# Performance work log

Hardware: AMD Instinct MI355X
Metric: run time of the kernel (lower is better)

The kernel has to match this reference:

```python
import jax, jax.numpy as jnp
import numpy as np

B, C, N, H = 4, 256, 1024, 8
D = C // H
EPS = 1e-5

def setup_inputs() -> dict:
    key = jax.random.key(0)
    ks = jax.random.split(key, 10)
    s = lambda k, shape: (jax.random.normal(k, shape, jnp.float32) * 0.02)
    return dict(
        node_embeds=jax.random.normal(ks[0], (B, C, N), jnp.float32),
        edge_embeds=jax.random.normal(ks[1], (B, N, N), jnp.float32),
        da_prior=jax.random.normal(ks[2], (B, N, C), jnp.float32),
        gamma=jnp.ones((C,), jnp.float32),
        beta=jnp.zeros((C,), jnp.float32),
        w_qkv=s(ks[3], (C, 3 * C)),            # Linear(node_dim, 3*node_dim), no bias
        w_proj=s(ks[4], (C, C)),
        b_proj=jnp.zeros((C,), jnp.float32),
        w_expand=s(ks[5], (H,)),               # Conv2d(1,H,1) weight (per-head scalar)
        b_expand=jnp.zeros((H,), jnp.float32),
        w_reduce=s(ks[6], (H,)),               # Conv2d(H,1,1) weight
        b_reduce=jnp.zeros((1,), jnp.float32),
        w_fc=s(ks[7], (1, C)),                 # Linear(edge_dim=1, node_dim)
        b_fc=jnp.zeros((C,), jnp.float32),
    )

def reference(node_embeds, edge_embeds, da_prior, gamma, beta, w_qkv,
              w_proj, b_proj, w_expand, b_expand, w_reduce, b_reduce, w_fc, b_fc):
    x = jnp.swapaxes(node_embeds, 1, 2)                       # [B,N,C]
    # einsum 'bnn,bnc->bnc': diagonal of edge matrix scales each node
    diag = jnp.diagonal(edge_embeds, axis1=1, axis2=2)        # [B,N]
    attned = diag[:, :, None] * x                             # [B,N,C]
    # einsum 'bnc,bca->bnc' with prior permuted [B,C,A]: multiply by sum over A
    prior_sum = da_prior.sum(axis=1)                          # [B,C]
    x = attned * prior_sum[:, None, :] + x                    # residual add
    # LayerNorm over channel dim
    mu = x.mean(-1, keepdims=True)
    var = x.var(-1, keepdims=True)
    ln = (x - mu) * jax.lax.rsqrt(var + EPS) * gamma + beta
    qkv = (ln @ w_qkv).reshape(B, N, 3, H, D)
    q = jnp.transpose(qkv[:, :, 0], (0, 2, 1, 3))             # [B,H,N,D]
    k = jnp.transpose(qkv[:, :, 1], (0, 2, 1, 3))
    v = jnp.transpose(qkv[:, :, 2], (0, 2, 1, 3))
    scale = D ** -0.5
    attn = jnp.einsum('bhnd,bhmd->bhnm', q, k) * scale        # [B,H,N,N]
    bias = edge_embeds[:, None] * w_expand[None, :, None, None] + b_expand[None, :, None, None]
    attn = attn + bias                                        # pre-softmax scores = residual
    a = jax.nn.softmax(attn, axis=-1)
    node = jnp.einsum('bhnm,bhmd->bnhd', a, v).reshape(B, N, C)
    # reduce conv over heads on (softmax + residual)
    edge = jnp.einsum('bhnm,h->bnm', a + attn, w_reduce) + b_reduce[0]  # [B,N,N]
    w = jax.nn.softmax(edge, axis=-1)
    wsum = (w * edge).sum(-1)                                 # [B,N]
    node = node + wsum[:, :, None] @ w_fc + b_fc              # fc: [B,N,1]@[1,C]
    node = node @ w_proj + b_proj
    return jnp.swapaxes(node, 1, 2), edge                     # ([B,C,N], [B,N,N])
```

## Files before the change

### kernel.cpp

```cpp
#include <hip/hip_runtime.h>
#include <math.h>

#define Bn 4
#define Cn 256
#define Nn 1024
#define Hn 8
#define Dn 32
#define BHND (Bn * Hn * Nn * Dn)
#define BHN  (Bn * Hn * Nn)

typedef short bf16x8 __attribute__((ext_vector_type(8)));
typedef float f32x4 __attribute__((ext_vector_type(4)));

__device__ inline unsigned f2bf_rn_bits(float x) {
  union { float f; unsigned u; } v; v.f = x;
  return (v.u + 0x7FFFu + ((v.u >> 16) & 1u)) >> 16;
}
__device__ inline float bfbits2f(unsigned b) {
  union { unsigned u; float f; } v; v.u = b << 16; return v.f;
}
__device__ inline void split_bf(float x, unsigned& hi, unsigned& lo) {
  hi = f2bf_rn_bits(x);
  lo = f2bf_rn_bits(x - bfbits2f(hi));
}
__device__ inline unsigned split_bf_trunc_pack(float x) {
  union { float f; unsigned u; } v; v.f = x;
  unsigned hi = v.u >> 16;
  union { unsigned u; float f; } hv; hv.u = hi << 16;
  union { float f; unsigned u; } r; r.f = x - hv.f;
  return hi | (r.u & 0xffff0000u);
}
__device__ inline void split4(const float4& a, float sc, short4& hs, short4& ls) {
  unsigned hb, lb;
  split_bf(a.x * sc, hb, lb); hs.x = (short)hb; ls.x = (short)lb;
  split_bf(a.y * sc, hb, lb); hs.y = (short)hb; ls.y = (short)lb;
  split_bf(a.z * sc, hb, lb); hs.z = (short)hb; ls.z = (short)lb;
  split_bf(a.w * sc, hb, lb); hs.w = (short)hb; ls.w = (short)lb;
}
__device__ inline void unpack_u32x8(const uint4& a, const uint4& b, bf16x8& hi, bf16x8& lo) {
  int4 h4, l4;
  h4.x = (int)((a.x & 0xffffu) | (a.y << 16));  l4.x = (int)((a.x >> 16) | (a.y & 0xffff0000u));
  h4.y = (int)((a.z & 0xffffu) | (a.w << 16));  l4.y = (int)((a.z >> 16) | (a.w & 0xffff0000u));
  h4.z = (int)((b.x & 0xffffu) | (b.y << 16));  l4.z = (int)((b.x >> 16) | (b.y & 0xffff0000u));
  h4.w = (int)((b.z & 0xffffu) | (b.w << 16));  l4.w = (int)((b.z >> 16) | (b.w & 0xffff0000u));
  hi = *(bf16x8*)&h4; lo = *(bf16x8*)&l4;
}

__global__ __launch_bounds__(256) void k_prior_part(const float* __restrict__ dap,
                                                    float* __restrict__ pp) {
  int bi = blockIdx.x;
  int b = bi >> 5, ch = bi & 31;
  int c = threadIdx.x;
  float s = 0.f;
  int n0 = ch * 32;
  for (int n = n0; n < n0 + 32; ++n) s += dap[(size_t)(b * Nn + n) * Cn + c];
  pp[(size_t)(b * 32 + ch) * Cn + c] = s;
}

__global__ __launch_bounds__(256) void k_prior_red(const float* __restrict__ pp,
                                                   float* __restrict__ prior) {
  int i = blockIdx.x * 256 + threadIdx.x;
  int b = i >> 8, c = i & 255;
  float s = 0.f;
  for (int ch = 0; ch < 32; ++ch) s += pp[(size_t)(b * 32 + ch) * Cn + c];
  prior[i] = s;
}

__global__ __launch_bounds__(256) void k_transpose(const float* __restrict__ ne,
                                                   float* __restrict__ xw) {
  __shared__ float tile[32][33];
  int bi = blockIdx.x;
  int b = bi >> 8, rem = bi & 255;
  int c0 = (rem >> 5) << 5;
  int n0 = (rem & 31) << 5;
  int tx = threadIdx.x & 31, ty = threadIdx.x >> 5;
#pragma unroll
  for (int i = 0; i < 4; ++i) {
    int c = c0 + ty + i * 8;
    tile[ty + i * 8][tx] = ne[(size_t)(b * Cn + c) * Nn + n0 + tx];
  }
  __syncthreads();
#pragma unroll
  for (int i = 0; i < 4; ++i) {
    int n = n0 + ty + i * 8;
    xw[(size_t)(b * Nn + n) * Cn + c0 + tx] = tile[tx][ty + i * 8];
  }
}

__global__ __launch_bounds__(256) void k_prep_ln(const float* __restrict__ xw,
                                                 const float* __restrict__ eg,
                                                 const float* __restrict__ prior,
                                                 const float* __restrict__ gamma,
                                                 const float* __restrict__ beta,
                                                 float* __restrict__ ln) {
  int bn = blockIdx.x;
  int b = bn >> 10, n = bn & 1023;
  int c = threadIdx.x;
  float x = xw[(size_t)bn * Cn + c];
  float dg = eg[(size_t)(b * Nn + n) * Nn + n];
  float x2 = x * (1.f + dg * prior[b * Cn + c]);
  float s = x2, qq = x2 * x2;
#pragma unroll
  for (int off = 32; off >= 1; off >>= 1) {
    s += __shfl_xor(s, off);
    qq += __shfl_xor(qq, off);
  }
  __shared__ float ss[4], sq[4];
  if ((c & 63) == 0) { ss[c >> 6] = s; sq[c >> 6] = qq; }
  __syncthreads();
  s = ss[0] + ss[1] + ss[2] + ss[3];
  qq = sq[0] + sq[1] + sq[2] + sq[3];
  float mu = s * (1.f / 256.f);
  float var = qq * (1.f / 256.f) - mu * mu;
  float r = rsqrtf(var + 1e-5f);
  ln[(size_t)bn * Cn + c] = (x2 - mu) * r * gamma[c] + beta[c];
}

__global__ __launch_bounds__(256) void k_qkv_gemm(const float* __restrict__ ln,
                                                  const float* __restrict__ wqkv,
                                                  short* __restrict__ q_hi,
                                                  short* __restrict__ q_lo,
                                                  short* __restrict__ k_hi,
                                                  short* __restrict__ k_lo,
                                                  short* __restrict__ vt_hi,
                                                  short* __restrict__ vt_lo) {
  __shared__ __align__(16) float at[16][68];
  __shared__ __align__(16) float bt[16][68];
  __shared__ float ct[64][65];
  int m0 = blockIdx.x * 64;
  int j0 = blockIdx.y * 64;
  int t = threadIdx.x;
  int tx = t & 15, ty = t >> 4;
  float4 acc[4] = {};
  for (int k0 = 0; k0 < 256; k0 += 16) {
    {
      int row = t >> 2, k4 = (t & 3) << 2;
      float4 a = *(const float4*)&ln[(size_t)(m0 + row) * 256 + k0 + k4];
      at[k4 + 0][row] = a.x; at[k4 + 1][row] = a.y;
      at[k4 + 2][row] = a.z; at[k4 + 3][row] = a.w;
      int rb = t >> 4, jb = (t & 15) << 2;
      *(float4*)&bt[rb][jb] = *(const float4*)&wqkv[(size_t)(k0 + rb) * 768 + j0 + jb];
    }
    __syncthreads();
#pragma unroll
    for (int kk = 0; kk < 16; ++kk) {
      float4 a4 = *(float4*)&at[kk][ty << 2];
      float4 b4 = *(float4*)&bt[kk][tx << 2];
      acc[0].x += a4.x * b4.x; acc[0].y += a4.x * b4.y; acc[0].z += a4.x * b4.z; acc[0].w += a4.x * b4.w;
      acc[1].x += a4.y * b4.x; acc[1].y += a4.y * b4.y; acc[1].z += a4.y * b4.z; acc[1].w += a4.y * b4.w;
      acc[2].x += a4.z * b4.x; acc[2].y += a4.z * b4.y; acc[2].z += a4.z * b4.z; acc[2].w += a4.z * b4.w;
      acc[3].x += a4.w * b4.x; acc[3].y += a4.w * b4.y; acc[3].z += a4.w * b4.z; acc[3].w += a4.w * b4.w;
    }
    __syncthreads();
  }
  int b = m0 >> 10, n0 = m0 & 1023;
  int three = (j0 + (tx << 2)) >> 8;
  const float scale = 0.17677669529663687f;
  if (three == 2) {
#pragma unroll
    for (int i = 0; i < 4; ++i) {
      ct[(ty << 2) + i][(tx << 2) + 0] = acc[i].x;
      ct[(ty << 2) + i][(tx << 2) + 1] = acc[i].y;
      ct[(ty << 2) + i][(tx << 2) + 2] = acc[i].z;
      ct[(ty << 2) + i][(tx << 2) + 3] = acc[i].w;
    }
    __syncthreads();
    int jl = t >> 2;
    int n4 = (t & 3) * 16;
    int rem = (j0 & 255) + jl;
    int h = rem >> 5, d = rem & 31;
    short hs[16], ls[16];
#pragma unroll
    for (int u = 0; u < 16; ++u) {
      unsigned hb, lb;
      split_bf(ct[n4 + u][jl], hb, lb);
      hs[u] = (short)hb; ls[u] = (short)lb;
    }
    size_t ob = ((size_t)(b * Hn + h) * Dn + d) * Nn + n0 + n4;
    *(uint4*)&vt_hi[ob] = *(uint4*)&hs[0];
    *(uint4*)&vt_hi[ob + 8] = *(uint4*)&hs[8];
    *(uint4*)&vt_lo[ob] = *(uint4*)&ls[0];
    *(uint4*)&vt_lo[ob + 8] = *(uint4*)&ls[8];
  } else {
    int j = j0 + (tx << 2);
    int rem = j & 255, h = rem >> 5, dd = rem & 31;
    short* dst_hi = (three == 0) ? q_hi : k_hi;
    short* dst_lo = (three == 0) ? q_lo : k_lo;
    float sc = (three == 0) ? 1.0f : scale;
#pragma unroll
    for (int i = 0; i < 4; ++i) {
      int m = m0 + (ty << 2) + i;
      int bb = m >> 10, n = m & 1023;
      size_t base = (size_t)((bb * Hn + h) * Nn + n) * Dn + dd;
      short4 hs, ls; split4(acc[i], sc, hs, ls);
      *(short4*)&dst_hi[base] = hs; *(short4*)&dst_lo[base] = ls;
    }
  }
}

__global__ __launch_bounds__(256, 4) void k_attn_core(
    const short* __restrict__ q_hi, const short* __restrict__ q_lo,
    const short* __restrict__ k_hi, const short* __restrict__ k_lo,
    const short* __restrict__ vt_hi, const short* __restrict__ vt_lo,
    const float* __restrict__ eg,
    const float* __restrict__ w_expand, const float* __restrict__ b_expand,
    float* __restrict__ o_part, float* __restrict__ l_part) {
  __shared__ short kh[64 * 40];
  __shared__ short kl[64 * 40];
  __shared__ short vth[32 * 72];
  __shared__ short vtl[32 * 72];
  __shared__ unsigned pbuf[4][16 * 68];

  int blk = blockIdx.x;
  int mh = blk & 1;
  int nt = (blk >> 1) & 15;
  int h = (blk >> 5) & 7;
  int b = blk >> 8;
  int n0 = nt * 64;
  int t = threadIdx.x, wid = t >> 6, l = t & 63;
  int lr = l & 15, lq = l >> 4;

  const float we = w_expand[h], be = b_expand[h];
  size_t bhb = (size_t)(b * Hn + h) * Nn * Dn;
  const short* khg = k_hi + bhb;
  const short* klg = k_lo + bhb;
  const short* vhg = vt_hi + bhb;
  const short* vlg = vt_lo + bhb;

  bf16x8 qhi, qlo;
  {
    size_t qoff = bhb + (size_t)(n0 + wid * 16 + lr) * Dn + lq * 8;
    qhi = *(const bf16x8*)&q_hi[qoff];
    qlo = *(const bf16x8*)&q_lo[qoff];
  }

  f32x4 O0 = {0.f, 0.f, 0.f, 0.f}, O1 = {0.f, 0.f, 0.f, 0.f};
  float rowsum[4] = {0.f, 0.f, 0.f, 0.f};
  int nrow = n0 + wid * 16 + lq * 4;

  for (int ms = 0; ms < 8; ++ms) {
    int m0 = mh * 512 + ms * 64;
    float eb[4][4];
#pragma unroll
    for (int reg = 0; reg < 4; ++reg) {
      const float* ep = &eg[(size_t)(b * Nn + nrow + reg) * Nn + m0 + lr];
#pragma unroll
      for (int msub = 0; msub < 4; ++msub) eb[msub][reg] = ep[msub * 16];
    }
    __syncthreads();
    {
      int row = t >> 2, c = (t & 3) * 8;
      *(uint4*)&kh[row * 40 + c] = *(const uint4*)&khg[(size_t)(m0 + row) * Dn + c];
      *(uint4*)&kl[row * 40 + c] = *(const uint4*)&klg[(size_t)(m0 + row) * Dn + c];
      int d = t >> 3, cm = (t & 7) * 8;
      *(uint4*)&vth[d * 72 + cm] = *(const uint4*)&vhg[(size_t)d * Nn + m0 + cm];
      *(uint4*)&vtl[d * 72 + cm] = *(const uint4*)&vlg[(size_t)d * Nn + m0 + cm];
    }
    __syncthreads();

#pragma unroll
    for (int msub = 0; msub < 4; ++msub) {
      int mrow = msub * 16 + lr;
      bf16x8 bh8 = *(bf16x8*)&kh[mrow * 40 + lq * 8];
      bf16x8 bl8 = *(bf16x8*)&kl[mrow * 40 + lq * 8];
      f32x4 sacc = {0.f, 0.f, 0.f, 0.f};
      sacc = __builtin_amdgcn_mfma_f32_16x16x32_bf16(qlo, bh8, sacc, 0, 0, 0);
      sacc = __builtin_amdgcn_mfma_f32_16x16x32_bf16(qhi, bl8, sacc, 0, 0, 0);
      sacc = __builtin_amdgcn_mfma_f32_16x16x32_bf16(qhi, bh8, sacc, 0, 0, 0);
#pragma unroll
      for (int reg = 0; reg < 4; ++reg) {
        float s = sacc[reg] + eb[msub][reg] * we + be;
        float e = __expf(s);
        rowsum[reg] += e;
        pbuf[wid][(lq * 4 + reg) * 68 + msub * 16 + lr] = split_bf_trunc_pack(e);
      }
    }

#pragma unroll
    for (int mw = 0; mw < 2; ++mw) {
      uint4 pa = *(uint4*)&pbuf[wid][lr * 68 + mw * 32 + lq * 8];
      uint4 pb = *(uint4*)&pbuf[wid][lr * 68 + mw * 32 + lq * 8 + 4];
      bf16x8 ahi, alo;
      unpack_u32x8(pa, pb, ahi, alo);
      {
        bf16x8 vh8 = *(bf16x8*)&vth[lr * 72 + mw * 32 + lq * 8];
        bf16x8 vl8 = *(bf16x8*)&vtl[lr * 72 + mw * 32 + lq * 8];
        O0 = __builtin_amdgcn_mfma_f32_16x16x32_bf16(alo, vh8, O0, 0, 0, 0);
        O0 = __builtin_amdgcn_mfma_f32_16x16x32_bf16(ahi, vl8, O0, 0, 0, 0);
        O0 = __builtin_amdgcn_mfma_f32_16x16x32_bf16(ahi, vh8, O0, 0, 0, 0);
      }
      {
        bf16x8 vh8 = *(bf16x8*)&vth[(16 + lr) * 72 + mw * 32 + lq * 8];
        bf16x8 vl8 = *(bf16x8*)&vtl[(16 + lr) * 72 + mw * 32 + lq * 8];
        O1 = __builtin_amdgcn_mfma_f32_16x16x32_bf16(alo, vh8, O1, 0, 0, 0);
        O1 = __builtin_amdgcn_mfma_f32_16x16x32_bf16(ahi, vl8, O1, 0, 0, 0);
        O1 = __builtin_amdgcn_mfma_f32_16x16x32_bf16(ahi, vh8, O1, 0, 0, 0);
      }
    }
  }

#pragma unroll
  for (int reg = 0; reg < 4; ++reg) {
#pragma unroll
    for (int off = 1; off < 16; off <<= 1)
      rowsum[reg] += __shfl_xor(rowsum[reg], off);
  }
  size_t pbase = (size_t)mh * BHND + bhb;
#pragma unroll
  for (int reg = 0; reg < 4; ++reg) {
    int n = nrow + reg;
    o_part[pbase + (size_t)n * Dn + lr] = O0[reg];
    o_part[pbase + (size_t)n * Dn + 16 + lr] = O1[reg];
    if (lr == 0)
      l_part[(size_t)mh * BHN + (size_t)(b * Hn + h) * Nn + n] = rowsum[reg];
  }
}

__global__ __launch_bounds__(256) void k_stats(const float* __restrict__ l_part,
                                               float* __restrict__ stats) {
  int i = blockIdx.x * 256 + threadIdx.x;
  stats[i] = 1.0f / (l_part[i] + l_part[BHN + i]);
}

__global__ __launch_bounds__(256, 4) void k_edge_mfma(
    const short* __restrict__ q_hi, const short* __restrict__ q_lo,
    const short* __restrict__ k_hi, const short* __restrict__ k_lo,
    const float* __restrict__ eg, const float* __restrict__ stats,
    const float* __restrict__ w_expand, const float* __restrict__ b_expand,
    const float* __restrict__ w_reduce, const float* __restrict__ b_reduce,
    float* __restrict__ edge_out) {
  __shared__ short kh[64 * 40];
  __shared__ short kl[64 * 40];
  int blk = blockIdx.x;
  int mt = blk & 15;
  int nt = (blk >> 4) & 15;
  int b = blk >> 8;
  int n0 = nt * 64, m0 = mt * 64;
  int t = threadIdx.x, wid = t >> 6, l = t & 63;
  int lr = l & 15, lq = l >> 4;
  const float br = b_reduce[0];
  int nrow = n0 + wid * 16 + lq * 4;

  float eacc[4][4], ebias[4][4];
#pragma unroll
  for (int reg = 0; reg < 4; ++reg) {
    const float* ep = &eg[(size_t)(b * Nn + nrow + reg) * Nn + m0 + lr];
#pragma unroll
    for (int msub = 0; msub < 4; ++msub) {
      ebias[msub][reg] = ep[msub * 16];
      eacc[msub][reg] = br;
    }
  }

  for (int h = 0; h < Hn; ++h) {
    size_t bhb = (size_t)(b * Hn + h) * Nn * Dn;
    float we = w_expand[h], be = b_expand[h], wr = w_reduce[h];
    bf16x8 qhi, qlo;
    {
      size_t qoff = bhb + (size_t)(n0 + wid * 16 + lr) * Dn + lq * 8;
      qhi = *(const bf16x8*)&q_hi[qoff];
      qlo = *(const bf16x8*)&q_lo[qoff];
    }
    float invl[4];
#pragma unroll
    for (int reg = 0; reg < 4; ++reg)
      invl[reg] = stats[(size_t)(b * Hn + h) * Nn + nrow + reg];

    __syncthreads();
    {
      int row = t >> 2, c = (t & 3) * 8;
      *(uint4*)&kh[row * 40 + c] = *(const uint4*)&k_hi[bhb + (size_t)(m0 + row) * Dn + c];
      *(uint4*)&kl[row * 40 + c] = *(const uint4*)&k_lo[bhb + (size_t)(m0 + row) * Dn + c];
    }
    __syncthreads();
#pragma unroll
    for (int msub = 0; msub < 4; ++msub) {
      int mrow = msub * 16 + lr;
      bf16x8 bh8 = *(bf16x8*)&kh[mrow * 40 + lq * 8];
      bf16x8 bl8 = *(bf16x8*)&kl[mrow * 40 + lq * 8];
      f32x4 sacc = {0.f, 0.f, 0.f, 0.f};
      sacc = __builtin_amdgcn_mfma_f32_16x16x32_bf16(qlo, bh8, sacc, 0, 0, 0);
      sacc = __builtin_amdgcn_mfma_f32_16x16x32_bf16(qhi, bl8, sacc, 0, 0, 0);
      sacc = __builtin_amdgcn_mfma_f32_16x16x32_bf16(qhi, bh8, sacc, 0, 0, 0);
#pragma unroll
      for (int reg = 0; reg < 4; ++reg) {
        float s = sacc[reg] + ebias[msub][reg] * we + be;
        float p = __expf(s) * invl[reg];
        eacc[msub][reg] += wr * (p + s);
      }
    }
  }
#pragma unroll
  for (int msub = 0; msub < 4; ++msub)
#pragma unroll
    for (int reg = 0; reg < 4; ++reg)
      edge_out[(size_t)(b * Nn + nrow + reg) * Nn + m0 + msub * 16 + lr] = eacc[msub][reg];
}

__global__ __launch_bounds__(256) void k_edge_soft(const float* __restrict__ edge,
                                                   float* __restrict__ wsum) {
  int bn = blockIdx.x;
  int t = threadIdx.x;
  const float* row = edge + (size_t)bn * Nn;
  float4 e = *(const float4*)&row[t * 4];
  float mx = fmaxf(fmaxf(e.x, e.y), fmaxf(e.z, e.w));
#pragma unroll
  for (int off = 32; off >= 1; off >>= 1) mx = fmaxf(mx, __shfl_xor(mx, off));
  __shared__ float sm[4], sl[4], sw[4];
  if ((t & 63) == 0) sm[t >> 6] = mx;
  __syncthreads();
  mx = fmaxf(fmaxf(sm[0], sm[1]), fmaxf(sm[2], sm[3]));
  float p0 = __expf(e.x - mx), p1 = __expf(e.y - mx), p2 = __expf(e.z - mx), p3 = __expf(e.w - mx);
  float ls = p0 + p1 + p2 + p3;
  float ws = p0 * e.x + p1 * e.y + p2 * e.z + p3 * e.w;
#pragma unroll
  for (int off = 32; off >= 1; off >>= 1) { ls += __shfl_xor(ls, off); ws += __shfl_xor(ws, off); }
  if ((t & 63) == 0) { sl[t >> 6] = ls; sw[t >> 6] = ws; }
  __syncthreads();
  if (t == 0) {
    float L = sl[0] + sl[1] + sl[2] + sl[3];
    float Wv = sw[0] + sw[1] + sw[2] + sw[3];
    wsum[bn] = Wv / L;
  }
}

__global__ __launch_bounds__(256) void k_proj_gemm(const float* __restrict__ o_part,
                                                   const float* __restrict__ stats,
                                                   const float* __restrict__ wsum,
                                                   const float* __restrict__ wfc,
                                                   const float* __restrict__ bfc,
                                                   const float* __restrict__ wproj,
                                                   const float* __restrict__ bproj,
                                                   float* __restrict__ out) {
  __shared__ __align__(16) float at[16][68];
  __shared__ __align__(16) float bt[16][68];
  __shared__ float ct[64][65];
  int m0 = blockIdx.x * 64;
  int j0 = blockIdx.y * 64;
  int t = threadIdx.x;
  int tx = t & 15, ty = t >> 4;
  float4 acc[4] = {};
  for (int k0 = 0; k0 < 256; k0 += 16) {
    {
      int row = t >> 2, k4 = (t & 3) << 2;
      int m = m0 + row;
      int bb = m >> 10, n = m & 1023;
      int c = k0 + k4;
      int h = c >> 5, dd = c & 31;
      float wsm = wsum[m];
      size_t ob = ((size_t)(bb * Hn + h) * Nn + n) * Dn + dd;
      float4 oa = *(const float4*)&o_part[ob];
      float4 oc = *(const float4*)&o_part[BHND + ob];
      float inv = stats[(size_t)(bb * Hn + h) * Nn + n];
      float4 a;
      a.x = (oa.x + oc.x) * inv + wsm * wfc[c + 0] + bfc[c + 0];
      a.y = (oa.y + oc.y) * inv + wsm * wfc[c + 1] + bfc[c + 1];
      a.z = (oa.z + oc.z) * inv + wsm * wfc[c + 2] + bfc[c + 2];
      a.w = (oa.w + oc.w) * inv + wsm * wfc[c + 3] + bfc[c + 3];
      at[k4 + 0][row] = a.x; at[k4 + 1][row] = a.y;
      at[k4 + 2][row] = a.z; at[k4 + 3][row] = a.w;
      int rb = t >> 4, jb = (t & 15) << 2;
      *(float4*)&bt[rb][jb] = *(const float4*)&wproj[(size_t)(k0 + rb) * 256 + j0 + jb];
    }
    __syncthreads();
#pragma unroll
    for (int kk = 0; kk < 16; ++kk) {
      float4 a4 = *(float4*)&at[kk][ty << 2];
      float4 b4 = *(float4*)&bt[kk][tx << 2];
      acc[0].x += a4.x * b4.x; acc[0].y += a4.x * b4.y; acc[0].z += a4.x * b4.z; acc[0].w += a4.x * b4.w;
      acc[1].x += a4.y * b4.x; acc[1].y += a4.y * b4.y; acc[1].z += a4.y * b4.z; acc[1].w += a4.y * b4.w;
      acc[2].x += a4.z * b4.x; acc[2].y += a4.z * b4.y; acc[2].z += a4.z * b4.z; acc[2].w += a4.z * b4.w;
      acc[3].x += a4.w * b4.x; acc[3].y += a4.w * b4.y; acc[3].z += a4.w * b4.z; acc[3].w += a4.w * b4.w;
    }
    __syncthreads();
  }
#pragma unroll
  for (int i = 0; i < 4; ++i) {
    ct[(ty << 2) + i][(tx << 2) + 0] = acc[i].x + bproj[j0 + (tx << 2) + 0];
    ct[(ty << 2) + i][(tx << 2) + 1] = acc[i].y + bproj[j0 + (tx << 2) + 1];
    ct[(ty << 2) + i][(tx << 2) + 2] = acc[i].z + bproj[j0 + (tx << 2) + 2];
    ct[(ty << 2) + i][(tx << 2) + 3] = acc[i].w + bproj[j0 + (tx << 2) + 3];
  }
  __syncthreads();
  int b = m0 >> 10, n0 = m0 & 1023;
  int n4 = t & 15, c0i = t >> 4;
#pragma unroll
  for (int u = 0; u < 4; ++u) {
    int ci = c0i + u * 16;
    float4 val = { ct[(n4 << 2) + 0][ci], ct[(n4 << 2) + 1][ci],
                   ct[(n4 << 2) + 2][ci], ct[(n4 << 2) + 3][ci] };
    *(float4*)&out[(size_t)(b * Cn + j0 + ci) * Nn + n0 + (n4 << 2)] = val;
  }
}

extern "C" void kernel_launch(void* const* d_in, const int* in_sizes, int n_in,
                              void* d_out, int out_size, void* d_ws, size_t ws_size,
                              hipStream_t stream) {
  (void)in_sizes; (void)n_in; (void)out_size; (void)ws_size;
  const float* node_embeds = (const float*)d_in[0];
  const float* edge_embeds = (const float*)d_in[1];
  const float* da_prior    = (const float*)d_in[2];
  const float* gamma       = (const float*)d_in[3];
  const float* beta        = (const float*)d_in[4];
  const float* w_qkv       = (const float*)d_in[5];
  const float* w_proj      = (const float*)d_in[6];
  const float* b_proj      = (const float*)d_in[7];
  const float* w_expand    = (const float*)d_in[8];
  const float* b_expand    = (const float*)d_in[9];
  const float* w_reduce    = (const float*)d_in[10];
  const float* b_reduce    = (const float*)d_in[11];
  const float* w_fc        = (const float*)d_in[12];
  const float* b_fc        = (const float*)d_in[13];
  float* out_node = (float*)d_out;
  float* out_edge = out_node + (size_t)Bn * Cn * Nn;

  const size_t M = 1048576;
  float* W = (float*)d_ws;
  float* ws_x   = W;
  float* ws_ln  = W + M;
  float* o_part = W;
  short* vt_hi  = (short*)(W + 2 * M);
  short* vt_lo  = vt_hi + M;
  short* q_hi   = (short*)(W + 3 * M);
  short* q_lo   = q_hi + M;
  short* k_hi   = q_hi + 2 * M;
  short* k_lo   = q_hi + 3 * M;
  float* ws_pp    = W + 5 * M;
  float* ws_prior = ws_pp + Bn * 32 * Cn;
  float* ws_wsum  = ws_prior + Bn * Cn;
  float* ws_stats = ws_wsum + Bn * Nn;
  float* l_part   = ws_stats + BHN;

  k_prior_part<<<dim3(Bn * 32), dim3(256), 0, stream>>>(da_prior, ws_pp);
  k_prior_red<<<dim3(Bn), dim3(256), 0, stream>>>(ws_pp, ws_prior);
  k_transpose<<<dim3(Bn * 256), dim3(256), 0, stream>>>(node_embeds, ws_x);
  k_prep_ln<<<dim3(Bn * Nn), dim3(256), 0, stream>>>(ws_x, edge_embeds, ws_prior,
                                                     gamma, beta, ws_ln);
  k_qkv_gemm<<<dim3(64, 12), dim3(256), 0, stream>>>(ws_ln, w_qkv, q_hi, q_lo,
                                                     k_hi, k_lo, vt_hi, vt_lo);
  k_attn_core<<<dim3(Bn * Hn * 16 * 2), dim3(256), 0, stream>>>(
      q_hi, q_lo, k_hi, k_lo, vt_hi, vt_lo, edge_embeds, w_expand, b_expand,
      o_part, l_part);
  k_stats<<<dim3(BHN / 256), dim3(256), 0, stream>>>(l_part, ws_stats);
  k_edge_mfma<<<dim3(Bn * 16 * 16), dim3(256), 0, stream>>>(
      q_hi, q_lo, k_hi, k_lo, edge_embeds, ws_stats, w_expand, b_expand,
      w_reduce, b_reduce, out_edge);
  k_edge_soft<<<dim3(Bn * Nn), dim3(256), 0, stream>>>(out_edge, ws_wsum);
  k_proj_gemm<<<dim3(64, 4), dim3(256), 0, stream>>>(o_part, ws_stats, ws_wsum,
                                                     w_fc, b_fc, w_proj, b_proj,
                                                     out_node);
}
```

Baseline: 200.2 us.

## Fuse edge softmax into edge kernel, MFMA split-bf16 QKV GEMM, inline stats

The fp32 SIMT QKV GEMM becomes a three-pass split-bf16 MFMA GEMM. LayerNorm now emits hi/lo bf16 directly, and a new pre-kernel transposes and splits w_qkv. The separate edge-softmax pass, which re-read the full edge matrix, is replaced by per-tile exp-sum partials computed in the edge MFMA epilogue, followed by a small reduction kernel. The k_stats kernel is removed and its reciprocal is computed inline where needed. The fused softmax drops the max subtraction, so it could overflow on inputs with large edge values.

Measured after the change: 206.2 us. +3.0%, slower.

```diff
diff --git a/kernel.cpp b/kernel.cpp
--- a/kernel.cpp
+++ b/kernel.cpp
@@ -29,13 +29,6 @@
   union { unsigned u; float f; } hv; hv.u = hi << 16;
   union { float f; unsigned u; } r; r.f = x - hv.f;
   return hi | (r.u & 0xffff0000u);
-}
-__device__ inline void split4(const float4& a, float sc, short4& hs, short4& ls) {
-  unsigned hb, lb;
-  split_bf(a.x * sc, hb, lb); hs.x = (short)hb; ls.x = (short)lb;
-  split_bf(a.y * sc, hb, lb); hs.y = (short)hb; ls.y = (short)lb;
-  split_bf(a.z * sc, hb, lb); hs.z = (short)hb; ls.z = (short)lb;
-  split_bf(a.w * sc, hb, lb); hs.w = (short)hb; ls.w = (short)lb;
 }
 __device__ inline void unpack_u32x8(const uint4& a, const uint4& b, bf16x8& hi, bf16x8& lo) {
   int4 h4, l4;
@@ -87,12 +80,34 @@
   }
 }
 
+__global__ __launch_bounds__(256) void k_split_wt(const float* __restrict__ w,
+                                                  short* __restrict__ wt_h,
+                                                  short* __restrict__ wt_l) {
+  __shared__ float tile[32][33];
+  int bi = blockIdx.x;
+  int j0 = (bi >> 3) << 5;
+  int k0 = (bi & 7) << 5;
+  int tx = threadIdx.x & 31, ty = threadIdx.x >> 5;
+#pragma unroll
+  for (int i = 0; i < 4; ++i)
+    tile[ty + i * 8][tx] = w[(size_t)(k0 + ty + i * 8) * 768 + j0 + tx];
+  __syncthreads();
+#pragma unroll
+  for (int i = 0; i < 4; ++i) {
+    float v = tile[tx][ty + i * 8];
+    unsigned hb, lb; split_bf(v, hb, lb);
+    wt_h[(size_t)(j0 + ty + i * 8) * 256 + k0 + tx] = (short)hb;
+    wt_l[(size_t)(j0 + ty + i * 8) * 256 + k0 + tx] = (short)lb;
+  }
+}
+
 __global__ __launch_bounds__(256) void k_prep_ln(const float* __restrict__ xw,
                                                  const float* __restrict__ eg,
                                                  const float* __restrict__ prior,
                                                  const float* __restrict__ gamma,
                                                  const float* __restrict__ beta,
-                                                 float* __restrict__ ln) {
+                                                 short* __restrict__ ln_h,
+                                                 short* __restrict__ ln_l) {
   int bn = blockIdx.x;
   int b = bn >> 10, n = bn & 1023;
   int c = threadIdx.x;
@@ -113,58 +128,51 @@
   float mu = s * (1.f / 256.f);
   float var = qq * (1.f / 256.f) - mu * mu;
   float r = rsqrtf(var + 1e-5f);
-  ln[(size_t)bn * Cn + c] = (x2 - mu) * r * gamma[c] + beta[c];
-}
-
-__global__ __launch_bounds__(256) void k_qkv_gemm(const float* __restrict__ ln,
-                                                  const float* __restrict__ wqkv,
-                                                  short* __restrict__ q_hi,
-                                                  short* __restrict__ q_lo,
-                                                  short* __restrict__ k_hi,
-                                                  short* __restrict__ k_lo,
-                                                  short* __restrict__ vt_hi,
-                                                  short* __restrict__ vt_lo) {
-  __shared__ __align__(16) float at[16][68];
-  __shared__ __align__(16) float bt[16][68];
+  float v = (x2 - mu) * r * gamma[c] + beta[c];
+  unsigned hb, lb; split_bf(v, hb, lb);
+  ln_h[(size_t)bn * Cn + c] = (short)hb;
+  ln_l[(size_t)bn * Cn + c] = (short)lb;
+}
+
+__global__ __launch_bounds__(256) void k_qkv_mfma(
+    const short* __restrict__ ln_h, const short* __restrict__ ln_l,
+    const short* __restrict__ wt_h, const short* __restrict__ wt_l,
+    short* __restrict__ q_hi, short* __restrict__ q_lo,
+    short* __restrict__ k_hi, short* __restrict__ k_lo,
+    short* __restrict__ vt_hi, short* __restrict__ vt_lo) {
   __shared__ float ct[64][65];
   int m0 = blockIdx.x * 64;
   int j0 = blockIdx.y * 64;
-  int t = threadIdx.x;
-  int tx = t & 15, ty = t >> 4;
-  float4 acc[4] = {};
-  for (int k0 = 0; k0 < 256; k0 += 16) {
-    {
-      int row = t >> 2, k4 = (t & 3) << 2;
-      float4 a = *(const float4*)&ln[(size_t)(m0 + row) * 256 + k0 + k4];
-      at[k4 + 0][row] = a.x; at[k4 + 1][row] = a.y;
-      at[k4 + 2][row] = a.z; at[k4 + 3][row] = a.w;
-      int rb = t >> 4, jb = (t & 15) << 2;
-      *(float4*)&bt[rb][jb] = *(const float4*)&wqkv[(size_t)(k0 + rb) * 768 + j0 + jb];
-    }
-    __syncthreads();
-#pragma unroll
-    for (int kk = 0; kk < 16; ++kk) {
-      float4 a4 = *(float4*)&at[kk][ty << 2];
-      float4 b4 = *(float4*)&bt[kk][tx << 2];
-      acc[0].x += a4.x * b4.x; acc[0].y += a4.x * b4.y; acc[0].z += a4.x * b4.z; acc[0].w += a4.x * b4.w;
-      acc[1].x += a4.y * b4.x; acc[1].y += a4.y * b4.y; acc[1].z += a4.y * b4.z; acc[1].w += a4.y * b4.w;
-      acc[2].x += a4.z * b4.x; acc[2].y += a4.z * b4.y; acc[2].z += a4.z * b4.z; acc[2].w += a4.z * b4.w;
-      acc[3].x += a4.w * b4.x; acc[3].y += a4.w * b4.y; acc[3].z += a4.w * b4.z; acc[3].w += a4.w * b4.w;
-    }
-    __syncthreads();
-  }
+  int t = threadIdx.x, wid = t >> 6, l = t & 63;
+  int lr = l & 15, lq = l >> 4;
+  f32x4 acc[4] = {};
+  const short* ah_p = ln_h + (size_t)(m0 + wid * 16 + lr) * 256 + lq * 8;
+  const short* al_p = ln_l + (size_t)(m0 + wid * 16 + lr) * 256 + lq * 8;
+  const short* bh_p = wt_h + (size_t)(j0 + lr) * 256 + lq * 8;
+  const short* bl_p = wt_l + (size_t)(j0 + lr) * 256 + lq * 8;
+#pragma unroll 2
+  for (int k0 = 0; k0 < 256; k0 += 32) {
+    bf16x8 ah = *(const bf16x8*)&ah_p[k0];
+    bf16x8 al = *(const bf16x8*)&al_p[k0];
+#pragma unroll
+    for (int js = 0; js < 4; ++js) {
+      bf16x8 bh = *(const bf16x8*)&bh_p[js * 16 * 256 + k0];
+      bf16x8 bl = *(const bf16x8*)&bl_p[js * 16 * 256 + k0];
+      acc[js] = __builtin_amdgcn_mfma_f32_16x16x32_bf16(al, bh, acc[js], 0, 0, 0);
+      acc[js] = __builtin_amdgcn_mfma_f32_16x16x32_bf16(ah, bl, acc[js], 0, 0, 0);
+      acc[js] = __builtin_amdgcn_mfma_f32_16x16x32_bf16(ah, bh, acc[js], 0, 0, 0);
+    }
+  }
+#pragma unroll
+  for (int js = 0; js < 4; ++js)
+#pragma unroll
+    for (int reg = 0; reg < 4; ++reg)
+      ct[wid * 16 + lq * 4 + reg][js * 16 + lr] = acc[js][reg];
+  __syncthreads();
   int b = m0 >> 10, n0 = m0 & 1023;
-  int three = (j0 + (tx << 2)) >> 8;
+  int three = j0 >> 8;
   const float scale = 0.17677669529663687f;
   if (three == 2) {
-#pragma unroll
-    for (int i = 0; i < 4; ++i) {
-      ct[(ty << 2) + i][(tx << 2) + 0] = acc[i].x;
-      ct[(ty << 2) + i][(tx << 2) + 1] = acc[i].y;
-      ct[(ty << 2) + i][(tx << 2) + 2] = acc[i].z;
-      ct[(ty << 2) + i][(tx << 2) + 3] = acc[i].w;
-    }
-    __syncthreads();
     int jl = t >> 2;
     int n4 = (t & 3) * 16;
     int rem = (j0 & 255) + jl;
@@ -182,19 +190,25 @@
     *(uint4*)&vt_lo[ob] = *(uint4*)&ls[0];
     *(uint4*)&vt_lo[ob + 8] = *(uint4*)&ls[8];
   } else {
-    int j = j0 + (tx << 2);
-    int rem = j & 255, h = rem >> 5, dd = rem & 31;
-    short* dst_hi = (three == 0) ? q_hi : k_hi;
-    short* dst_lo = (three == 0) ? q_lo : k_lo;
+    int m_l = t & 63, half = t >> 6;
+    int rem = (j0 & 255) + half * 16;
+    int h = rem >> 5, ddb = rem & 31;
+    int n = n0 + m_l;
     float sc = (three == 0) ? 1.0f : scale;
-#pragma unroll
-    for (int i = 0; i < 4; ++i) {
-      int m = m0 + (ty << 2) + i;
-      int bb = m >> 10, n = m & 1023;
-      size_t base = (size_t)((bb * Hn + h) * Nn + n) * Dn + dd;
-      short4 hs, ls; split4(acc[i], sc, hs, ls);
-      *(short4*)&dst_hi[base] = hs; *(short4*)&dst_lo[base] = ls;
-    }
+    short* dh = three ? k_hi : q_hi;
+    short* dl = three ? k_lo : q_lo;
+    short hs[16], ls[16];
+#pragma unroll
+    for (int u = 0; u < 16; ++u) {
+      unsigned hb, lb;
+      split_bf(ct[m_l][half * 16 + u] * sc, hb, lb);
+      hs[u] = (short)hb; ls[u] = (short)lb;
+    }
+    size_t base = ((size_t)((b * Hn + h) * Nn + n)) * Dn + ddb;
+    *(uint4*)&dh[base] = *(uint4*)&hs[0];
+    *(uint4*)&dh[base + 8] = *(uint4*)&hs[8];
+    *(uint4*)&dl[base] = *(uint4*)&ls[0];
+    *(uint4*)&dl[base + 8] = *(uint4*)&ls[8];
   }
 }
 
@@ -316,19 +330,14 @@
   }
 }
 
-__global__ __launch_bounds__(256) void k_stats(const float* __restrict__ l_part,
-                                               float* __restrict__ stats) {
-  int i = blockIdx.x * 256 + threadIdx.x;
-  stats[i] = 1.0f / (l_part[i] + l_part[BHN + i]);
-}
-
 __global__ __launch_bounds__(256, 4) void k_edge_mfma(
     const short* __restrict__ q_hi, const short* __restrict__ q_lo,
     const short* __restrict__ k_hi, const short* __restrict__ k_lo,
-    const float* __restrict__ eg, const float* __restrict__ stats,
+    const float* __restrict__ eg, const float* __restrict__ l_part,
     const float* __restrict__ w_expand, const float* __restrict__ b_expand,
     const float* __restrict__ w_reduce, const float* __restrict__ b_reduce,
-    float* __restrict__ edge_out) {
+    float* __restrict__ edge_out, float* __restrict__ pl_part,
+    float* __restrict__ pwe_part) {
   __shared__ short kh[64 * 40];
   __shared__ short kl[64 * 40];
   int blk = blockIdx.x;
@@ -363,8 +372,10 @@
     }
     float invl[4];
 #pragma unroll
-    for (int reg = 0; reg < 4; ++reg)
-      invl[reg] = stats[(size_t)(b * Hn + h) * Nn + nrow + reg];
+    for (int reg = 0; reg < 4; ++reg) {
+      size_t idx = (size_t)(b * Hn + h) * Nn + nrow + reg;
+      invl[reg] = 1.0f / (l_part[idx] + l_part[BHN + idx]);
+    }
 
     __syncthreads();
     {
@@ -395,37 +406,46 @@
 #pragma unroll
     for (int reg = 0; reg < 4; ++reg)
       edge_out[(size_t)(b * Nn + nrow + reg) * Nn + m0 + msub * 16 + lr] = eacc[msub][reg];
-}
-
-__global__ __launch_bounds__(256) void k_edge_soft(const float* __restrict__ edge,
-                                                   float* __restrict__ wsum) {
-  int bn = blockIdx.x;
-  int t = threadIdx.x;
-  const float* row = edge + (size_t)bn * Nn;
-  float4 e = *(const float4*)&row[t * 4];
-  float mx = fmaxf(fmaxf(e.x, e.y), fmaxf(e.z, e.w));
-#pragma unroll
-  for (int off = 32; off >= 1; off >>= 1) mx = fmaxf(mx, __shfl_xor(mx, off));
-  __shared__ float sm[4], sl[4], sw[4];
-  if ((t & 63) == 0) sm[t >> 6] = mx;
-  __syncthreads();
-  mx = fmaxf(fmaxf(sm[0], sm[1]), fmaxf(sm[2], sm[3]));
-  float p0 = __expf(e.x - mx), p1 = __expf(e.y - mx), p2 = __expf(e.z - mx), p3 = __expf(e.w - mx);
-  float ls = p0 + p1 + p2 + p3;
-  float ws = p0 * e.x + p1 * e.y + p2 * e.z + p3 * e.w;
-#pragma unroll
-  for (int off = 32; off >= 1; off >>= 1) { ls += __shfl_xor(ls, off); ws += __shfl_xor(ws, off); }
-  if ((t & 63) == 0) { sl[t >> 6] = ls; sw[t >> 6] = ws; }
-  __syncthreads();
-  if (t == 0) {
-    float L = sl[0] + sl[1] + sl[2] + sl[3];
-    float Wv = sw[0] + sw[1] + sw[2] + sw[3];
-    wsum[bn] = Wv / L;
-  }
+
+  float pl[4] = {0.f, 0.f, 0.f, 0.f}, pw[4] = {0.f, 0.f, 0.f, 0.f};
+#pragma unroll
+  for (int msub = 0; msub < 4; ++msub)
+#pragma unroll
+    for (int reg = 0; reg < 4; ++reg) {
+      float e = eacc[msub][reg];
+      float x = __expf(e);
+      pl[reg] += x;
+      pw[reg] += x * e;
+    }
+#pragma unroll
+  for (int reg = 0; reg < 4; ++reg) {
+#pragma unroll
+    for (int off = 1; off < 16; off <<= 1) {
+      pl[reg] += __shfl_xor(pl[reg], off);
+      pw[reg] += __shfl_xor(pw[reg], off);
+    }
+    if (lr == 0) {
+      int idx = mt * (Bn * Nn) + b * Nn + nrow + reg;
+      pl_part[idx] = pl[reg];
+      pwe_part[idx] = pw[reg];
+    }
+  }
+}
+
+__global__ __launch_bounds__(256) void k_edge_red(const float* __restrict__ pl,
+                                                  const float* __restrict__ pwe,
+                                                  float* __restrict__ wsum) {
+  int i = blockIdx.x * 256 + threadIdx.x;
+  float L = 0.f, Wv = 0.f;
+  for (int mt = 0; mt < 16; ++mt) {
+    L += pl[mt * (Bn * Nn) + i];
+    Wv += pwe[mt * (Bn * Nn) + i];
+  }
+  wsum[i] = Wv / L;
 }
 
 __global__ __launch_bounds__(256) void k_proj_gemm(const float* __restrict__ o_part,
-                                                   const float* __restrict__ stats,
+                                                   const float* __restrict__ l_part,
                                                    const float* __restrict__ wsum,
                                                    const float* __restrict__ wfc,
                                                    const float* __restrict__ bfc,
@@ -451,7 +471,8 @@
       size_t ob = ((size_t)(bb * Hn + h) * Nn + n) * Dn + dd;
       float4 oa = *(const float4*)&o_part[ob];
       float4 oc = *(const float4*)&o_part[BHND + ob];
-      float inv = stats[(size_t)(bb * Hn + h) * Nn + n];
+      size_t sidx = (size_t)(bb * Hn + h) * Nn + n;
+      float inv = 1.0f / (l_part[sidx] + l_part[BHN + sidx]);
       float4 a;
       a.x = (oa.x + oc.x) * inv + wsm * wfc[c + 0] + bfc[c + 0];
       a.y = (oa.y + oc.y) * inv + wsm * wfc[c + 1] + bfc[c + 1];
@@ -517,7 +538,8 @@
   const size_t M = 1048576;
   float* W = (float*)d_ws;
   float* ws_x   = W;
-  float* ws_ln  = W + M;
+  short* ln_hi  = (short*)(W + M);
+  short* ln_lo  = ln_hi + M;
   float* o_part = W;
   short* vt_hi  = (short*)(W + 2 * M);
   short* vt_lo  = vt_hi + M;
@@ -528,25 +550,29 @@
   float* ws_pp    = W + 5 * M;
   float* ws_prior = ws_pp + Bn * 32 * Cn;
   float* ws_wsum  = ws_prior + Bn * Cn;
-  float* ws_stats = ws_wsum + Bn * Nn;
-  float* l_part   = ws_stats + BHN;
-
+  float* l_part   = ws_wsum + Bn * Nn;
+  float* pl_part  = l_part + 2 * BHN;
+  float* pwe_part = pl_part + 16 * Bn * Nn;
+  short* wt_hi    = (short*)(pwe_part + 16 * Bn * Nn);
+  short* wt_lo    = wt_hi + 768 * 256;
+
+  k_split_wt<<<dim3(192), dim3(256), 0, stream>>>(w_qkv, wt_hi, wt_lo);
   k_prior_part<<<dim3(Bn * 32), dim3(256), 0, stream>>>(da_prior, ws_pp);
   k_prior_red<<<dim3(Bn), dim3(256), 0, stream>>>(ws_pp, ws_prior);
   k_transpose<<<dim3(Bn * 256), dim3(256), 0, stream>>>(node_embeds, ws_x);
   k_prep_ln<<<dim3(Bn * Nn), dim3(256), 0, stream>>>(ws_x, edge_embeds, ws_prior,
-                                                     gamma, beta, ws_ln);
-  k_qkv_gemm<<<dim3(64, 12), dim3(256), 0, stream>>>(ws_ln, w_qkv, q_hi, q_lo,
-                                                     k_hi, k_lo, vt_hi, vt_lo);
+                                                     gamma, beta, ln_hi, ln_lo);
+  k_qkv_mfma<<<dim3(64, 12), dim3(256), 0, stream>>>(ln_hi, ln_lo, wt_hi, wt_lo,
+                                                     q_hi, q_lo, k_hi, k_lo,
+                                                     vt_hi, vt_lo);
   k_attn_core<<<dim3(Bn * Hn * 16 * 2), dim3(256), 0, stream>>>(
       q_hi, q_lo, k_hi, k_lo, vt_hi, vt_lo, edge_embeds, w_expand, b_expand,
       o_part, l_part);
-  k_stats<<<dim3(BHN / 256), dim3(256), 0, stream>>>(l_part, ws_stats);
   k_edge_mfma<<<dim3(Bn * 16 * 16), dim3(256), 0, stream>>>(
-      q_hi, q_lo, k_hi, k_lo, edge_embeds, ws_stats, w_expand, b_expand,
-      w_reduce, b_reduce, out_edge);
-  k_edge_soft<<<dim3(Bn * Nn), dim3(256), 0, stream>>>(out_edge, ws_wsum);
-  k_proj_gemm<<<dim3(64, 4), dim3(256), 0, stream>>>(o_part, ws_stats, ws_wsum,
+      q_hi, q_lo, k_hi, k_lo, edge_embeds, l_part, w_expand, b_expand,
+      w_reduce, b_reduce, out_edge, pl_part, pwe_part);
+  k_edge_red<<<dim3(16), dim3(256), 0, stream>>>(pl_part, pwe_part, ws_wsum);
+  k_proj_gemm<<<dim3(64, 4), dim3(256), 0, stream>>>(o_part, l_part, ws_wsum,
                                                      w_fc, b_fc, w_proj, b_proj,
                                                      out_node);
 }
```
